# Performance work log

Measured on AMD Instinct MI355X. Metric: run time of the kernel, lower is better.

## Reference

```python
import jax, jax.numpy as jnp
import numpy as np

B, S, D = 2, 2048, 2048
HQ, HKV, HD = 16, 4, 128
EPS = 1e-8


def _rope_tables(seq_len, dim, base=10000.0):
    inv_freq = 1.0 / (base ** (jnp.arange(0, dim, 2, dtype=jnp.float32) / dim))
    freqs = jnp.outer(jnp.arange(seq_len, dtype=jnp.float32), inv_freq)  # S x dim/2
    emb = jnp.concatenate([freqs, freqs], axis=-1)  # S x dim
    return jnp.cos(emb), jnp.sin(emb)


def setup_inputs() -> dict:
    key = jax.random.key(0)
    ks = jax.random.split(key, 6)
    cos_theta, sin_theta = _rope_tables(S, HD)
    return {
        "x": jax.random.normal(ks[0], (B, S, D), dtype=jnp.float32),
        "Wq": jax.random.normal(ks[1], (D, HQ * HD), dtype=jnp.float32) * 0.02,
        "Wk": jax.random.normal(ks[2], (D, HKV * HD), dtype=jnp.float32) * 0.02,
        "Wv": jax.random.normal(ks[3], (D, HKV * HD), dtype=jnp.float32) * 0.02,
        "Wo": jax.random.normal(ks[4], (HQ * HD, D), dtype=jnp.float32) * 0.02,
        "q_norm_w": jnp.zeros((HD,), dtype=jnp.float32),
        "k_norm_w": jnp.zeros((HD,), dtype=jnp.float32),
        "cos_theta": cos_theta,
        "sin_theta": sin_theta,
        "padding_mask": jnp.zeros((B, S), dtype=bool),
        "window_size": 1024,
    }


def _rmsnorm(x, w):
    return x * jax.lax.rsqrt(jnp.mean(x * x, axis=-1, keepdims=True) + EPS) * (1.0 + w)


def _rotate_half(x):
    x1, x2 = jnp.split(x, 2, axis=-1)
    return jnp.concatenate([-x2, x1], axis=-1)


def _rope(x, cos_t, sin_t):
    # x: B x H x S x d; cos/sin: S x d
    return x * cos_t[None, None] + _rotate_half(x) * sin_t[None, None]


def reference(x, Wq, Wk, Wv, Wo, q_norm_w, k_norm_w, cos_theta, sin_theta, padding_mask, window_size):
    b, s, _ = x.shape
    scale = HD ** -0.5
    q = (x @ Wq).reshape(b, s, HQ, HD).transpose(0, 2, 1, 3)   # b,HQ,s,d
    k = (x @ Wk).reshape(b, s, HKV, HD).transpose(0, 2, 1, 3)  # b,HKV,s,d
    v = (x @ Wv).reshape(b, s, HKV, HD).transpose(0, 2, 1, 3)
    q = _rope(_rmsnorm(q, q_norm_w), cos_theta[:s], sin_theta[:s])
    k = _rope(_rmsnorm(k, k_norm_w), cos_theta[:s], sin_theta[:s])

    # causal & sliding window & padding mask
    qi = jnp.arange(s)[:, None]
    ki = jnp.arange(s)[None, :]
    mask = (qi >= ki) & ((qi - ki) <= window_size)          # s x s
    pad = padding_mask[:, :, None] | padding_mask[:, None, :]  # b x s x s
    mask = mask[None] & ~pad                                 # b x s x s

    g = HQ // HKV
    qg = q.reshape(b, HKV, g, s, HD)
    scores = jnp.einsum('bngqd,bnkd->bngqk', qg, k) * scale  # b,HKV,g,s,s
    scores = jnp.where(mask[:, None, None], scores, -jnp.inf)
    attn = jax.nn.softmax(scores, axis=-1)
    out = jnp.einsum('bngqk,bnkd->bngqd', attn, v)
    out = out.reshape(b, HQ, s, HD).transpose(0, 2, 1, 3).reshape(b, s, HQ * HD)
    return out @ Wo
```

## Files before the change

### kernel.cpp

```cpp
#include <hip/hip_runtime.h>

typedef __attribute__((ext_vector_type(4))) float f32x4;
typedef __attribute__((ext_vector_type(8))) __bf16 bf16x8;
typedef __attribute__((ext_vector_type(4))) __bf16 bf16x4;

__device__ __forceinline__ void gload_lds16(const __bf16* g, __bf16* l) {
  __builtin_amdgcn_global_load_lds(
      (const __attribute__((address_space(1))) unsigned int*)(g),
      (__attribute__((address_space(3))) unsigned int*)(l), 16, 0, 0);
}

__global__ __launch_bounds__(256) void prep(
    const float* __restrict__ Wq, const float* __restrict__ Wk,
    const float* __restrict__ Wv, const float* __restrict__ Wo,
    const float4* __restrict__ x, const unsigned long long* __restrict__ pad,
    __bf16* __restrict__ Wqkvt, __bf16* __restrict__ Wot,
    bf16x4* __restrict__ xb, unsigned char* __restrict__ pad64) {
  const int bx = blockIdx.x, by = blockIdx.y;
  const int tx = threadIdx.x, ty = threadIdx.y;
  const int tid = ty * 32 + tx;
  if (bx >= 160) {
    int i = ((bx - 160) * 64 + by) * 256 + tid;
    float4 v = x[i];
    bf16x4 o = {(__bf16)v.x, (__bf16)v.y, (__bf16)v.z, (__bf16)v.w};
    xb[i] = o;
    return;
  }
  if (bx == 0 && by == 0 && tid < 64) {
    unsigned long long acc = 0;
#pragma unroll
    for (int i = 0; i < 8; ++i) acc |= pad[tid * 8 + i];
    pad64[tid] = (acc != 0) ? 1 : 0;
  }
  __shared__ float t[32][33];
  const float* src; __bf16* dst; int ss, c0;
  if (bx < 64)      { src = Wq; dst = Wqkvt;                       ss = 2048; c0 = bx * 32; }
  else if (bx < 80) { src = Wk; dst = Wqkvt + (size_t)2048 * 2048; ss = 512;  c0 = (bx - 64) * 32; }
  else if (bx < 96) { src = Wv; dst = Wqkvt + (size_t)2560 * 2048; ss = 512;  c0 = (bx - 80) * 32; }
  else              { src = Wo; dst = Wot;                         ss = 2048; c0 = (bx - 96) * 32; }
  const int r0 = by * 32;
#pragma unroll
  for (int i = ty; i < 32; i += 8)
    t[i][tx] = src[(size_t)(r0 + i) * ss + c0 + tx];
  __syncthreads();
#pragma unroll
  for (int i = ty; i < 32; i += 8)
    dst[(size_t)(c0 + i) * 2048 + r0 + tx] = (__bf16)t[tx][i];
}

__global__ __launch_bounds__(256) void gemm_qkv(
    const __bf16* __restrict__ A, const __bf16* __restrict__ Bt,
    __bf16* __restrict__ Qb, __bf16* __restrict__ Kb, __bf16* __restrict__ Vt) {
  __shared__ __align__(16) __bf16 smem[128 * 136];
  __bf16* As = smem;
  __bf16* Bs = smem + 128 * 32;
  __bf16* stage = smem;
  const int K = 2048;
  const int tid = threadIdx.x;
  const int lane = tid & 63;
  const int c15 = lane & 15, quad = lane >> 4;
  const int wm = ((tid >> 6) & 1) * 64;
  const int wn = (tid >> 7) * 64;
  const int jb = blockIdx.x;
  const int m0 = blockIdx.y * 128, n0 = jb * 128;
  const int wbase = tid & 192;

  f32x4 acc[4][4] = {};

  const int row0 = tid >> 2, cc0 = (tid & 3) * 8;
  const int row1 = (tid + 256) >> 2;
  const __bf16* a0 = A + (size_t)(m0 + row0) * K + cc0;
  const __bf16* a1 = A + (size_t)(m0 + row1) * K + cc0;
  const __bf16* b0 = Bt + (size_t)(n0 + row0) * K + cc0;
  const __bf16* b1 = Bt + (size_t)(n0 + row1) * K + cc0;
  __bf16* lA0 = As + (size_t)wbase * 8;
  __bf16* lA1 = As + (size_t)(256 + wbase) * 8;
  __bf16* lB0 = Bs + (size_t)wbase * 8;
  __bf16* lB1 = Bs + (size_t)(256 + wbase) * 8;

  for (int k0 = 0; k0 < K; k0 += 32) {
    gload_lds16(a0 + k0, lA0);
    gload_lds16(a1 + k0, lA1);
    gload_lds16(b0 + k0, lB0);
    gload_lds16(b1 + k0, lB1);
    __syncthreads();
    bf16x8 af[4], bfr[4];
#pragma unroll
    for (int i = 0; i < 4; ++i) {
      af[i]  = *(const bf16x8*)(As + (wm + i * 16 + c15) * 32 + quad * 8);
      bfr[i] = *(const bf16x8*)(Bs + (wn + i * 16 + c15) * 32 + quad * 8);
    }
#pragma unroll
    for (int i = 0; i < 4; ++i)
#pragma unroll
      for (int j = 0; j < 4; ++j)
        acc[i][j] = __builtin_amdgcn_mfma_f32_16x16x32_bf16(af[i], bfr[j], acc[i][j], 0, 0, 0);
    __syncthreads();
  }

  const int b = m0 >> 11;
  const int s0 = m0 & 2047;
  const int orow = tid >> 4, ocol = (tid & 15) * 8;

  if (jb >= 20) {
#pragma unroll
    for (int j = 0; j < 4; ++j) {
      int d = wn + j * 16 + c15;
#pragma unroll
      for (int i = 0; i < 4; ++i) {
        int sl = wm + i * 16 + quad * 4;
        bf16x4 o = {(__bf16)acc[i][j][0], (__bf16)acc[i][j][1],
                    (__bf16)acc[i][j][2], (__bf16)acc[i][j][3]};
        *(bf16x4*)(stage + (size_t)d * 136 + sl) = o;
      }
    }
    __syncthreads();
    __bf16* VtH = Vt + (((size_t)b * 4 + (jb - 20)) * 128) * 2048;
#pragma unroll
    for (int p = 0; p < 8; ++p) {
      int d = p * 16 + orow;
      *(bf16x8*)(VtH + (size_t)d * 2048 + s0 + ocol) =
          *(const bf16x8*)(stage + (size_t)d * 136 + ocol);
    }
    return;
  }

#pragma unroll
  for (int i = 0; i < 4; ++i)
#pragma unroll
    for (int j = 0; j < 4; ++j)
#pragma unroll
      for (int r = 0; r < 4; ++r)
        stage[(size_t)(wm + i * 16 + quad * 4 + r) * 136 + wn + j * 16 + c15] =
            (__bf16)acc[i][j][r];
  __syncthreads();
  __bf16* dstH = (jb < 16) ? Qb + (((size_t)b * 16 + jb) * 2048) * 128
                           : Kb + (((size_t)b * 4 + (jb - 16)) * 2048) * 128;
#pragma unroll
  for (int p = 0; p < 8; ++p) {
    int sl = p * 16 + orow;
    *(bf16x8*)(dstH + (size_t)(s0 + sl) * 128 + ocol) =
        *(const bf16x8*)(stage + (size_t)sl * 136 + ocol);
  }
}

__global__ __launch_bounds__(256) void norm_rope(
    __bf16* __restrict__ Qb, __bf16* __restrict__ Kb,
    const float* __restrict__ qw, const float* __restrict__ kw,
    const float* __restrict__ cosT, const float* __restrict__ sinT) {
  const int tid = threadIdx.x, w = tid >> 6, lane = tid & 63;
  const int v = blockIdx.x * 4 + w;
  const bool isQ = v < 65536;
  __bf16* base = isQ ? Qb + (size_t)v * 128 : Kb + (size_t)(v - 65536) * 128;
  const int s = v & 2047;
  float x1 = (float)base[lane], x2 = (float)base[lane + 64];
  float ss = x1 * x1 + x2 * x2;
#pragma unroll
  for (int d = 32; d; d >>= 1) ss += __shfl_xor(ss, d);
  float rn = rsqrtf(ss * (1.0f / 128.0f) + 1e-8f);
  const float* wt = isQ ? qw : kw;
  float n1 = x1 * rn * (1.0f + wt[lane]);
  float n2 = x2 * rn * (1.0f + wt[lane + 64]);
  float c1 = cosT[s * 128 + lane], c2 = cosT[s * 128 + 64 + lane];
  float s1 = sinT[s * 128 + lane], s2 = sinT[s * 128 + 64 + lane];
  const float QSC = 0.08838834764831845f * 1.4426950408889634f;
  float post = isQ ? QSC : 1.0f;
  base[lane]      = (__bf16)((n1 * c1 - n2 * s1) * post);
  base[lane + 64] = (__bf16)((n2 * c2 + n1 * s2) * post);
}

__global__ __launch_bounds__(256) void gemm_bt(const __bf16* __restrict__ A,
                                               const __bf16* __restrict__ Bt,
                                               float* __restrict__ C,
                                               int M, int N, int K) {
  __shared__ __align__(16) __bf16 As[128 * 32];
  __shared__ __align__(16) __bf16 Bs[128 * 32];
  const int tid = threadIdx.x;
  const int lane = tid & 63;
  const int c15 = lane & 15, quad = lane >> 4;
  const int wm = ((tid >> 6) & 1) * 64;
  const int wn = (tid >> 7) * 64;
  const int m0 = blockIdx.y * 128, n0 = blockIdx.x * 128;
  const int wbase = tid & 192;

  f32x4 acc[4][4] = {};

  const int row0 = tid >> 2, cc0 = (tid & 3) * 8;
  const int row1 = (tid + 256) >> 2;
  const __bf16* a0 = A + (size_t)(m0 + row0) * K + cc0;
  const __bf16* a1 = A + (size_t)(m0 + row1) * K + cc0;
  const __bf16* b0 = Bt + (size_t)(n0 + row0) * K + cc0;
  const __bf16* b1 = Bt + (size_t)(n0 + row1) * K + cc0;
  __bf16* lA0 = As + (size_t)wbase * 8;
  __bf16* lA1 = As + (size_t)(256 + wbase) * 8;
  __bf16* lB0 = Bs + (size_t)wbase * 8;
  __bf16* lB1 = Bs + (size_t)(256 + wbase) * 8;

  for (int k0 = 0; k0 < K; k0 += 32) {
    gload_lds16(a0 + k0, lA0);
    gload_lds16(a1 + k0, lA1);
    gload_lds16(b0 + k0, lB0);
    gload_lds16(b1 + k0, lB1);
    __syncthreads();
    bf16x8 af[4], bfr[4];
#pragma unroll
    for (int i = 0; i < 4; ++i) {
      af[i]  = *(const bf16x8*)(As + (wm + i * 16 + c15) * 32 + quad * 8);
      bfr[i] = *(const bf16x8*)(Bs + (wn + i * 16 + c15) * 32 + quad * 8);
    }
#pragma unroll
    for (int i = 0; i < 4; ++i)
#pragma unroll
      for (int j = 0; j < 4; ++j)
        acc[i][j] = __builtin_amdgcn_mfma_f32_16x16x32_bf16(af[i], bfr[j], acc[i][j], 0, 0, 0);
    __syncthreads();
  }

#pragma unroll
  for (int i = 0; i < 4; ++i) {
    int r0 = m0 + wm + i * 16 + quad * 4;
#pragma unroll
    for (int j = 0; j < 4; ++j) {
      int cc = n0 + wn + j * 16 + c15;
#pragma unroll
      for (int r = 0; r < 4; ++r)
        C[(size_t)(r0 + r) * N + cc] = acc[i][j][r];
    }
  }
}

__global__ __launch_bounds__(256) void attn(
    const __bf16* __restrict__ Qb, const __bf16* __restrict__ Kb,
    const __bf16* __restrict__ Vt, const unsigned char* __restrict__ pad,
    const unsigned char* __restrict__ pad64, const int* __restrict__ winp,
    __bf16* __restrict__ O) {
  const int S = 2048;
  __shared__ __align__(16) __bf16 Ks[64 * 128];
  __shared__ __align__(16) __bf16 Vs[128 * 64];
  __shared__ __align__(16) __bf16 Ps[4 * 16 * 72];
  const int tid = threadIdx.x, w = tid >> 6, lane = tid & 63;
  const int c15 = lane & 15, quad = lane >> 4;
  const int q0 = (gridDim.x - 1 - blockIdx.x) * 16;
  const int kv = blockIdx.y, b = blockIdx.z;
  const int h = kv * 4 + w;
  const int W = *winp;
  const unsigned char* padb = pad + (size_t)b * S;
  const unsigned char* pad64b = pad64 + b * 32;
  const __bf16* Qh = Qb + (((size_t)b * 16 + h) * S) * 128;
  const __bf16* Kh = Kb + (((size_t)b * 4 + kv) * S) * 128;
  const __bf16* Vh = Vt + (((size_t)b * 4 + kv) * 128) * (size_t)S;
  __bf16* Pw = Ps + w * 16 * 72;

  bf16x8 qf[4];
#pragma unroll
  for (int c = 0; c < 4; ++c)
    qf[c] = *(const bf16x8*)(Qh + (size_t)(q0 + c15) * 128 + c * 32 + quad * 8);

  f32x4 acc[8] = {};
  float lsum[4] = {0.f, 0.f, 0.f, 0.f};

  const int krow_i = lane >> 4, kch = lane & 15;
  const int vrow_i = lane >> 3, vch = lane & 7;

  int kb0 = q0 - W; if (kb0 < 0) kb0 = 0; kb0 &= ~63;

  for (int kb = kb0; kb <= q0 + 15; kb += 64) {
    __syncthreads();
#pragma unroll
    for (int i = 0; i < 4; ++i) {
      int row = w * 16 + i * 4 + krow_i;
      gload_lds16(Kh + (size_t)(kb + row) * 128 + ((kch ^ (row & 15)) * 8),
                  Ks + (w * 16 + i * 4) * 128);
    }
#pragma unroll
    for (int i = 0; i < 4; ++i) {
      int row = w * 32 + i * 8 + vrow_i;
      gload_lds16(Vh + (size_t)row * S + kb + ((vch ^ (row & 7)) * 8),
                  Vs + (w * 32 + i * 8) * 64);
    }
    __syncthreads();

    f32x4 sf[4];
#pragma unroll
    for (int nb = 0; nb < 4; ++nb) {
      f32x4 cacc = {};
#pragma unroll
      for (int c = 0; c < 4; ++c) {
        bf16x8 kf = *(const bf16x8*)(Ks + (nb * 16 + c15) * 128 + (((c * 4 + quad) ^ c15) * 8));
        cacc = __builtin_amdgcn_mfma_f32_16x16x32_bf16(qf[c], kf, cacc, 0, 0, 0);
      }
      sf[nb] = cacc;
    }

    const bool fast = (kb + 63 <= q0) && (q0 + 15 - kb <= W) && (pad64b[kb >> 6] == 0);
    if (fast) {
#pragma unroll
      for (int r = 0; r < 4; ++r) {
        float p0 = exp2f(sf[0][r]), p1 = exp2f(sf[1][r]);
        float p2 = exp2f(sf[2][r]), p3 = exp2f(sf[3][r]);
        lsum[r] += (p0 + p1) + (p2 + p3);
        int pr = (quad * 4 + r) * 72 + c15;
        Pw[pr] = (__bf16)p0; Pw[pr + 16] = (__bf16)p1;
        Pw[pr + 32] = (__bf16)p2; Pw[pr + 48] = (__bf16)p3;
      }
    } else {
#pragma unroll
      for (int r = 0; r < 4; ++r) {
        const int qi = q0 + quad * 4 + r;
        float p[4];
#pragma unroll
        for (int nb = 0; nb < 4; ++nb) {
          int ki = kb + nb * 16 + c15;
          bool ok = (ki <= qi) && ((qi - ki) <= W) && (padb[ki] == 0);
          float e = exp2f(sf[nb][r]);
          p[nb] = ok ? e : 0.0f;
        }
        lsum[r] += (p[0] + p[1]) + (p[2] + p[3]);
        int pr = (quad * 4 + r) * 72 + c15;
        Pw[pr] = (__bf16)p[0]; Pw[pr + 16] = (__bf16)p[1];
        Pw[pr + 32] = (__bf16)p[2]; Pw[pr + 48] = (__bf16)p[3];
      }
    }

    bf16x8 pf0 = *(const bf16x8*)(Pw + c15 * 72 + quad * 8);
    bf16x8 pf1 = *(const bf16x8*)(Pw + c15 * 72 + 32 + quad * 8);
#pragma unroll
    for (int nb = 0; nb < 8; ++nb) {
      int row = nb * 16 + c15;
      bf16x8 vf0 = *(const bf16x8*)(Vs + row * 64 + ((quad ^ (c15 & 7)) * 8));
      bf16x8 vf1 = *(const bf16x8*)(Vs + row * 64 + (((4 + quad) ^ (c15 & 7)) * 8));
      acc[nb] = __builtin_amdgcn_mfma_f32_16x16x32_bf16(pf0, vf0, acc[nb], 0, 0, 0);
      acc[nb] = __builtin_amdgcn_mfma_f32_16x16x32_bf16(pf1, vf1, acc[nb], 0, 0, 0);
    }
  }

#pragma unroll
  for (int r = 0; r < 4; ++r) {
    lsum[r] += __shfl_xor(lsum[r], 1);
    lsum[r] += __shfl_xor(lsum[r], 2);
    lsum[r] += __shfl_xor(lsum[r], 4);
    lsum[r] += __shfl_xor(lsum[r], 8);
  }
  float inv[4];
#pragma unroll
  for (int r = 0; r < 4; ++r) inv[r] = 1.0f / lsum[r];
#pragma unroll
  for (int nb = 0; nb < 8; ++nb)
#pragma unroll
    for (int r = 0; r < 4; ++r) {
      size_t idx = ((size_t)b * S + q0 + quad * 4 + r) * 2048 + h * 128 + nb * 16 + c15;
      O[idx] = (__bf16)(acc[nb][r] * inv[r]);
    }
}

extern "C" void kernel_launch(void* const* d_in, const int* in_sizes, int n_in,
                              void* d_out, int out_size, void* d_ws, size_t ws_size,
                              hipStream_t stream) {
  const float* x    = (const float*)d_in[0];
  const float* Wq   = (const float*)d_in[1];
  const float* Wk   = (const float*)d_in[2];
  const float* Wv   = (const float*)d_in[3];
  const float* Wo   = (const float*)d_in[4];
  const float* qw   = (const float*)d_in[5];
  const float* kw   = (const float*)d_in[6];
  const float* cosT = (const float*)d_in[7];
  const float* sinT = (const float*)d_in[8];
  const unsigned char* pad = (const unsigned char*)d_in[9];
  const int* win    = (const int*)d_in[10];

  char* ws = (char*)d_ws;
  __bf16* xb    = (__bf16*)(ws + 0);
  __bf16* Wqkvt = (__bf16*)(ws + 16777216);
  __bf16* Wot   = (__bf16*)(ws + 29360128);
  __bf16* Qb    = (__bf16*)(ws + 37748736);
  __bf16* Kb    = (__bf16*)(ws + 54525952);
  __bf16* Vt    = (__bf16*)(ws + 58720256);
  __bf16* Ob    = (__bf16*)(ws + 62914560);
  unsigned char* pad64 = (unsigned char*)(ws + 79691776);

  prep<<<dim3(288, 64, 1), dim3(32, 8, 1), 0, stream>>>(
      Wq, Wk, Wv, Wo, (const float4*)x, (const unsigned long long*)pad,
      Wqkvt, Wot, (bf16x4*)xb, pad64);

  gemm_qkv<<<dim3(24, 32, 1), 256, 0, stream>>>(xb, Wqkvt, Qb, Kb, Vt);

  norm_rope<<<20480, 256, 0, stream>>>(Qb, Kb, qw, kw, cosT, sinT);

  attn<<<dim3(128, 4, 2), 256, 0, stream>>>(Qb, Kb, Vt, pad, pad64, win, Ob);

  gemm_bt<<<dim3(16, 32, 1), 256, 0, stream>>>(Ob, Wot, (float*)d_out, 4096, 2048, 2048);
}
```

Measured before the change: 339.4 us.

## Process two 16-row query tiles per wave in attention to reuse K/V tiles

Each wave in the attention kernel now handles 32 query rows (two 16-row MFMA tiles) instead of 16. Every K and V fragment loaded from LDS, and every K/V tile staged from global memory, therefore serves twice as many queries. The grid is halved to 64 blocks along the query axis. This doubles accumulator and Q-fragment registers per thread, which may lower occupancy, and with fewer blocks there may be less parallelism and worse load balance across CUs.

New measurement: 340.7 us. No clear change (+0.4%).

```diff
diff --git a/kernel.cpp b/kernel.cpp
--- a/kernel.cpp
+++ b/kernel.cpp
@@ -237,10 +237,10 @@
   const int S = 2048;
   __shared__ __align__(16) __bf16 Ks[64 * 128];
   __shared__ __align__(16) __bf16 Vs[128 * 64];
-  __shared__ __align__(16) __bf16 Ps[4 * 16 * 72];
+  __shared__ __align__(16) __bf16 Ps[4 * 32 * 72];
   const int tid = threadIdx.x, w = tid >> 6, lane = tid & 63;
   const int c15 = lane & 15, quad = lane >> 4;
-  const int q0 = (gridDim.x - 1 - blockIdx.x) * 16;
+  const int q0 = (gridDim.x - 1 - blockIdx.x) * 32;
   const int kv = blockIdx.y, b = blockIdx.z;
   const int h = kv * 4 + w;
   const int W = *winp;
@@ -249,22 +249,24 @@
   const __bf16* Qh = Qb + (((size_t)b * 16 + h) * S) * 128;
   const __bf16* Kh = Kb + (((size_t)b * 4 + kv) * S) * 128;
   const __bf16* Vh = Vt + (((size_t)b * 4 + kv) * 128) * (size_t)S;
-  __bf16* Pw = Ps + w * 16 * 72;
-
-  bf16x8 qf[4];
-#pragma unroll
-  for (int c = 0; c < 4; ++c)
-    qf[c] = *(const bf16x8*)(Qh + (size_t)(q0 + c15) * 128 + c * 32 + quad * 8);
-
-  f32x4 acc[8] = {};
-  float lsum[4] = {0.f, 0.f, 0.f, 0.f};
+  __bf16* Pw = Ps + w * 32 * 72;
+
+  bf16x8 qf[2][4];
+#pragma unroll
+  for (int qt = 0; qt < 2; ++qt)
+#pragma unroll
+    for (int c = 0; c < 4; ++c)
+      qf[qt][c] = *(const bf16x8*)(Qh + (size_t)(q0 + qt * 16 + c15) * 128 + c * 32 + quad * 8);
+
+  f32x4 acc[2][8] = {};
+  float lsum[2][4] = {};
 
   const int krow_i = lane >> 4, kch = lane & 15;
   const int vrow_i = lane >> 3, vch = lane & 7;
 
   int kb0 = q0 - W; if (kb0 < 0) kb0 = 0; kb0 &= ~63;
 
-  for (int kb = kb0; kb <= q0 + 15; kb += 64) {
+  for (int kb = kb0; kb <= q0 + 31; kb += 64) {
     __syncthreads();
 #pragma unroll
     for (int i = 0; i < 4; ++i) {
@@ -280,77 +282,88 @@
     }
     __syncthreads();
 
-    f32x4 sf[4];
-#pragma unroll
-    for (int nb = 0; nb < 4; ++nb) {
-      f32x4 cacc = {};
+    f32x4 sf[2][4] = {};
+#pragma unroll
+    for (int nb = 0; nb < 4; ++nb)
 #pragma unroll
       for (int c = 0; c < 4; ++c) {
         bf16x8 kf = *(const bf16x8*)(Ks + (nb * 16 + c15) * 128 + (((c * 4 + quad) ^ c15) * 8));
-        cacc = __builtin_amdgcn_mfma_f32_16x16x32_bf16(qf[c], kf, cacc, 0, 0, 0);
+        sf[0][nb] = __builtin_amdgcn_mfma_f32_16x16x32_bf16(qf[0][c], kf, sf[0][nb], 0, 0, 0);
+        sf[1][nb] = __builtin_amdgcn_mfma_f32_16x16x32_bf16(qf[1][c], kf, sf[1][nb], 0, 0, 0);
       }
-      sf[nb] = cacc;
-    }
-
-    const bool fast = (kb + 63 <= q0) && (q0 + 15 - kb <= W) && (pad64b[kb >> 6] == 0);
+
+    const bool fast = (kb + 63 <= q0) && (q0 + 31 - kb <= W) && (pad64b[kb >> 6] == 0);
     if (fast) {
 #pragma unroll
-      for (int r = 0; r < 4; ++r) {
-        float p0 = exp2f(sf[0][r]), p1 = exp2f(sf[1][r]);
-        float p2 = exp2f(sf[2][r]), p3 = exp2f(sf[3][r]);
-        lsum[r] += (p0 + p1) + (p2 + p3);
-        int pr = (quad * 4 + r) * 72 + c15;
-        Pw[pr] = (__bf16)p0; Pw[pr + 16] = (__bf16)p1;
-        Pw[pr + 32] = (__bf16)p2; Pw[pr + 48] = (__bf16)p3;
-      }
+      for (int qt = 0; qt < 2; ++qt)
+#pragma unroll
+        for (int r = 0; r < 4; ++r) {
+          float p0 = exp2f(sf[qt][0][r]), p1 = exp2f(sf[qt][1][r]);
+          float p2 = exp2f(sf[qt][2][r]), p3 = exp2f(sf[qt][3][r]);
+          lsum[qt][r] += (p0 + p1) + (p2 + p3);
+          int pr = (qt * 16 + quad * 4 + r) * 72 + c15;
+          Pw[pr] = (__bf16)p0; Pw[pr + 16] = (__bf16)p1;
+          Pw[pr + 32] = (__bf16)p2; Pw[pr + 48] = (__bf16)p3;
+        }
     } else {
 #pragma unroll
-      for (int r = 0; r < 4; ++r) {
-        const int qi = q0 + quad * 4 + r;
-        float p[4];
-#pragma unroll
-        for (int nb = 0; nb < 4; ++nb) {
-          int ki = kb + nb * 16 + c15;
-          bool ok = (ki <= qi) && ((qi - ki) <= W) && (padb[ki] == 0);
-          float e = exp2f(sf[nb][r]);
-          p[nb] = ok ? e : 0.0f;
+      for (int qt = 0; qt < 2; ++qt)
+#pragma unroll
+        for (int r = 0; r < 4; ++r) {
+          const int qi = q0 + qt * 16 + quad * 4 + r;
+          float p[4];
+#pragma unroll
+          for (int nb = 0; nb < 4; ++nb) {
+            int ki = kb + nb * 16 + c15;
+            bool ok = (ki <= qi) && ((qi - ki) <= W) && (padb[ki] == 0);
+            float e = exp2f(sf[qt][nb][r]);
+            p[nb] = ok ? e : 0.0f;
+          }
+          lsum[qt][r] += (p[0] + p[1]) + (p[2] + p[3]);
+          int pr = (qt * 16 + quad * 4 + r) * 72 + c15;
+          Pw[pr] = (__bf16)p[0]; Pw[pr + 16] = (__bf16)p[1];
+          Pw[pr + 32] = (__bf16)p[2]; Pw[pr + 48] = (__bf16)p[3];
         }
-        lsum[r] += (p[0] + p[1]) + (p[2] + p[3]);
-        int pr = (quad * 4 + r) * 72 + c15;
-        Pw[pr] = (__bf16)p[0]; Pw[pr + 16] = (__bf16)p[1];
-        Pw[pr + 32] = (__bf16)p[2]; Pw[pr + 48] = (__bf16)p[3];
-      }
-    }
-
-    bf16x8 pf0 = *(const bf16x8*)(Pw + c15 * 72 + quad * 8);
-    bf16x8 pf1 = *(const bf16x8*)(Pw + c15 * 72 + 32 + quad * 8);
+    }
+
+    bf16x8 pf[2][2];
+#pragma unroll
+    for (int qt = 0; qt < 2; ++qt) {
+      pf[qt][0] = *(const bf16x8*)(Pw + (qt * 16 + c15) * 72 + quad * 8);
+      pf[qt][1] = *(const bf16x8*)(Pw + (qt * 16 + c15) * 72 + 32 + quad * 8);
+    }
 #pragma unroll
     for (int nb = 0; nb < 8; ++nb) {
       int row = nb * 16 + c15;
       bf16x8 vf0 = *(const bf16x8*)(Vs + row * 64 + ((quad ^ (c15 & 7)) * 8));
       bf16x8 vf1 = *(const bf16x8*)(Vs + row * 64 + (((4 + quad) ^ (c15 & 7)) * 8));
-      acc[nb] = __builtin_amdgcn_mfma_f32_16x16x32_bf16(pf0, vf0, acc[nb], 0, 0, 0);
-      acc[nb] = __builtin_amdgcn_mfma_f32_16x16x32_bf16(pf1, vf1, acc[nb], 0, 0, 0);
-    }
-  }
-
-#pragma unroll
-  for (int r = 0; r < 4; ++r) {
-    lsum[r] += __shfl_xor(lsum[r], 1);
-    lsum[r] += __shfl_xor(lsum[r], 2);
-    lsum[r] += __shfl_xor(lsum[r], 4);
-    lsum[r] += __shfl_xor(lsum[r], 8);
-  }
-  float inv[4];
-#pragma unroll
-  for (int r = 0; r < 4; ++r) inv[r] = 1.0f / lsum[r];
-#pragma unroll
-  for (int nb = 0; nb < 8; ++nb)
+#pragma unroll
+      for (int qt = 0; qt < 2; ++qt) {
+        acc[qt][nb] = __builtin_amdgcn_mfma_f32_16x16x32_bf16(pf[qt][0], vf0, acc[qt][nb], 0, 0, 0);
+        acc[qt][nb] = __builtin_amdgcn_mfma_f32_16x16x32_bf16(pf[qt][1], vf1, acc[qt][nb], 0, 0, 0);
+      }
+    }
+  }
+
+#pragma unroll
+  for (int qt = 0; qt < 2; ++qt)
 #pragma unroll
     for (int r = 0; r < 4; ++r) {
-      size_t idx = ((size_t)b * S + q0 + quad * 4 + r) * 2048 + h * 128 + nb * 16 + c15;
-      O[idx] = (__bf16)(acc[nb][r] * inv[r]);
-    }
+      lsum[qt][r] += __shfl_xor(lsum[qt][r], 1);
+      lsum[qt][r] += __shfl_xor(lsum[qt][r], 2);
+      lsum[qt][r] += __shfl_xor(lsum[qt][r], 4);
+      lsum[qt][r] += __shfl_xor(lsum[qt][r], 8);
+      lsum[qt][r] = 1.0f / lsum[qt][r];
+    }
+#pragma unroll
+  for (int qt = 0; qt < 2; ++qt)
+#pragma unroll
+    for (int nb = 0; nb < 8; ++nb)
+#pragma unroll
+      for (int r = 0; r < 4; ++r) {
+        size_t idx = ((size_t)b * S + q0 + qt * 16 + quad * 4 + r) * 2048 + h * 128 + nb * 16 + c15;
+        O[idx] = (__bf16)(acc[qt][nb][r] * lsum[qt][r]);
+      }
 }
 
 extern "C" void kernel_launch(void* const* d_in, const int* in_sizes, int n_in,
@@ -386,7 +399,7 @@
 
   norm_rope<<<20480, 256, 0, stream>>>(Qb, Kb, qw, kw, cosT, sinT);
 
-  attn<<<dim3(128, 4, 2), 256, 0, stream>>>(Qb, Kb, Vt, pad, pad64, win, Ob);
+  attn<<<dim3(64, 4, 2), 256, 0, stream>>>(Qb, Kb, Vt, pad, pad64, win, Ob);
 
   gemm_bt<<<dim3(16, 32, 1), 256, 0, stream>>>(Ob, Wot, (float*)d_out, 4096, 2048, 2048);
 }
```
